# Performance work log

Measured on AMD Instinct MI355X. Metric: run time of the kernel, lower is better.

## Reference

```python
import jax, jax.numpy as jnp
import numpy as np

B, L, H, W_MAX, N_CLASSES = 32, 2048, 768, 512, 16


def setup_inputs() -> dict:
    key = jax.random.key(0)
    k_enc, k_len, k_w1, k_w2 = jax.random.split(key, 4)
    encoder_output = jax.random.normal(k_enc, (B, L, H), dtype=jnp.float32)
    # Ragged word spans: word lengths in [1, 8], consecutive spans via exclusive cumsum.
    lengths = jax.random.randint(k_len, (B, W_MAX), 1, 9)
    ends = jnp.cumsum(lengths, axis=1).astype(jnp.int32)
    starts = (ends - lengths).astype(jnp.int32)
    # Spans running past L become invalid (mask=0), matching the original's guard.
    W1 = jax.random.normal(k_w1, (H, H // 2), dtype=jnp.float32) * 0.02
    b1 = jnp.zeros((H // 2,), dtype=jnp.float32)
    W2 = jax.random.normal(k_w2, (H // 2, N_CLASSES), dtype=jnp.float32) * 0.02
    b2 = jnp.zeros((N_CLASSES,), dtype=jnp.float32)
    return {"encoder_output": encoder_output, "starts": starts, "ends": ends,
            "W1": W1, "b1": b1, "W2": W2, "b2": b2}


def reference(encoder_output, starts, ends, W1, b1, W2, b2):
    Bq, Lq, Hq = encoder_output.shape
    # Validity guard identical to original: s < L and e <= L and s < e
    valid = (starts < Lq) & (ends <= Lq) & (starts < ends)          # (B, W)
    mask = valid.astype(jnp.float32)
    # Prefix sums over sequence dim (zero-prepended): (B, L+1, H)
    csum = jnp.concatenate(
        [jnp.zeros((Bq, 1, Hq), encoder_output.dtype),
         jnp.cumsum(encoder_output, axis=1)], axis=1)
    s_idx = jnp.clip(starts, 0, Lq)[:, :, None]                      # (B, W, 1)
    e_idx = jnp.clip(ends, 0, Lq)[:, :, None]
    span_sum = (jnp.take_along_axis(csum, e_idx, axis=1)
                - jnp.take_along_axis(csum, s_idx, axis=1))          # (B, W, H)
    counts = jnp.maximum(ends - starts, 1).astype(encoder_output.dtype)[:, :, None]
    pooled = jnp.where(valid[:, :, None], span_sum / counts, 0.0)    # (B, W, H)
    # MLP head (dropout is identity in eval mode); torch GELU default = exact erf
    h = jax.nn.gelu(pooled @ W1 + b1, approximate=False)
    logits = h @ W2 + b2                                             # (B, W, n_classes)
    return logits, mask
```

## Files before the change

kernel.cpp:

```cpp
#include <hip/hip_runtime.h>
#include <hip/hip_bf16.h>

#define B_  32
#define L_  2048
#define H_  768
#define W_  512
#define NC_ 16
#define HH_ 384

typedef __attribute__((ext_vector_type(8))) __bf16 bf16x8;
typedef __attribute__((ext_vector_type(4))) float floatx4;

static __device__ __forceinline__ unsigned short f2bf(float x) {
    union { float f; unsigned u; } v; v.f = x;
    unsigned r = v.u + 0x7FFF + ((v.u >> 16) & 1);
    return (unsigned short)(r >> 16);
}

__global__ void k_convert_w1(const float* __restrict__ W1, unsigned short* __restrict__ w1t) {
    int idx = blockIdx.x * 256 + threadIdx.x;
    int n = idx / H_;
    int k = idx - n * H_;
    w1t[idx] = f2bf(W1[k * HH_ + n]);
}

__global__ void k_pool(const float* __restrict__ enc, const int* __restrict__ starts,
                       const int* __restrict__ ends, unsigned short* __restrict__ pooled,
                       float* __restrict__ mask) {
    int bw = blockIdx.x;
    int t  = threadIdx.x;
    int s = starts[bw], e = ends[bw];
    bool valid = (s < L_) && (e <= L_) && (s < e);
    float4 acc = make_float4(0.f, 0.f, 0.f, 0.f);
    if (valid) {
        int b = bw >> 9;
        const float4* base = (const float4*)(enc + (size_t)b * L_ * H_);
        float inv = 1.0f / (float)(e - s);
        for (int r = s; r < e; ++r) {
            float4 v = base[r * (H_ / 4) + t];
            acc.x += v.x; acc.y += v.y; acc.z += v.z; acc.w += v.w;
        }
        acc.x *= inv; acc.y *= inv; acc.z *= inv; acc.w *= inv;
    }
    ushort4 o;
    o.x = f2bf(acc.x); o.y = f2bf(acc.y); o.z = f2bf(acc.z); o.w = f2bf(acc.w);
    *(ushort4*)(pooled + (size_t)bw * H_ + t * 4) = o;
    if (t == 0) mask[bw] = valid ? 1.0f : 0.0f;
}

#define BM  64
#define BK  64
#define LDA 72
#define LDB 72
#define LDH 388

__global__ __launch_bounds__(512) void k_mlp(
    const unsigned short* __restrict__ pooled,
    const unsigned short* __restrict__ w1t,
    const float* __restrict__ b1,
    const float* __restrict__ W2,
    const float* __restrict__ b2,
    float* __restrict__ out)
{
    __shared__ float smem[BM * LDH];
    unsigned short* sA = (unsigned short*)smem;
    unsigned short* sB = (unsigned short*)smem + BM * LDA;

    const int tid  = threadIdx.x;
    const int wave = tid >> 6, lane = tid & 63;
    const int wm = wave >> 2, wn = wave & 3;
    const int lr = lane & 15, lk = lane >> 4;

    const int m0 = blockIdx.x * BM;

    floatx4 acc[2][6];
    #pragma unroll
    for (int i = 0; i < 2; ++i)
        #pragma unroll
        for (int j = 0; j < 6; ++j) acc[i][j] = {0.f, 0.f, 0.f, 0.f};

    const int srow = tid >> 3;
    const int sseg = (tid & 7) * 8;

    for (int kt = 0; kt < 12; ++kt) {
        const int k0 = kt * BK;
        {
            bf16x8 v = *(const bf16x8*)(pooled + (size_t)(m0 + srow) * H_ + k0 + sseg);
            *(bf16x8*)(sA + srow * LDA + sseg) = v;
        }
        #pragma unroll
        for (int p = 0; p < 6; ++p) {
            int nrow = srow + p * 64;
            bf16x8 v = *(const bf16x8*)(w1t + (size_t)nrow * H_ + k0 + sseg);
            *(bf16x8*)(sB + nrow * LDB + sseg) = v;
        }
        __syncthreads();
        #pragma unroll
        for (int kk = 0; kk < 2; ++kk) {
            bf16x8 af[2], bfr[6];
            #pragma unroll
            for (int mi = 0; mi < 2; ++mi)
                af[mi] = *(const bf16x8*)(sA + (wm * 32 + mi * 16 + lr) * LDA + kk * 32 + lk * 8);
            #pragma unroll
            for (int ni = 0; ni < 6; ++ni)
                bfr[ni] = *(const bf16x8*)(sB + (wn * 96 + ni * 16 + lr) * LDB + kk * 32 + lk * 8);
            #pragma unroll
            for (int mi = 0; mi < 2; ++mi)
                #pragma unroll
                for (int ni = 0; ni < 6; ++ni)
                    acc[mi][ni] = __builtin_amdgcn_mfma_f32_16x16x32_bf16(
                        af[mi], bfr[ni], acc[mi][ni], 0, 0, 0);
        }
        __syncthreads();
    }

    #pragma unroll
    for (int mi = 0; mi < 2; ++mi) {
        #pragma unroll
        for (int ni = 0; ni < 6; ++ni) {
            int col = wn * 96 + ni * 16 + lr;
            float bias = b1[col];
            #pragma unroll
            for (int r = 0; r < 4; ++r) {
                int row = wm * 32 + mi * 16 + lk * 4 + r;
                float x = acc[mi][ni][r] + bias;
                float g = 0.5f * x * (1.0f + erff(x * 0.70710678118654752f));
                smem[row * LDH + col] = g;
            }
        }
    }
    __syncthreads();

    const int r = tid >> 3;
    const int c = tid & 7;
    float s0 = b2[c], s1 = b2[c + 8];
    const float* hrow = smem + r * LDH;
    #pragma unroll 4
    for (int k = 0; k < HH_; ++k) {
        float hv = hrow[k];
        s0 += hv * W2[k * NC_ + c];
        s1 += hv * W2[k * NC_ + c + 8];
    }
    float* orow = out + (size_t)(m0 + r) * NC_;
    orow[c] = s0;
    orow[c + 8] = s1;
}

extern "C" void kernel_launch(void* const* d_in, const int* in_sizes, int n_in,
                              void* d_out, int out_size, void* d_ws, size_t ws_size,
                              hipStream_t stream) {
    const float* enc    = (const float*)d_in[0];
    const int*   starts = (const int*)d_in[1];
    const int*   ends   = (const int*)d_in[2];
    const float* W1     = (const float*)d_in[3];
    const float* b1     = (const float*)d_in[4];
    const float* W2     = (const float*)d_in[5];
    const float* b2     = (const float*)d_in[6];
    float* out = (float*)d_out;

    unsigned short* w1t    = (unsigned short*)d_ws;
    unsigned short* pooled = w1t + (size_t)HH_ * H_;
    float* mask = out + (size_t)B_ * W_ * NC_;

    hipLaunchKernelGGL(k_convert_w1, dim3((HH_ * H_) / 256), dim3(256), 0, stream, W1, w1t);
    hipLaunchKernelGGL(k_pool, dim3(B_ * W_), dim3(192), 0, stream, enc, starts, ends, pooled, mask);
    hipLaunchKernelGGL(k_mlp, dim3((B_ * W_) / BM), dim3(512), 0, stream, pooled, w1t, b1, W2, b2, out);
}
```

Baseline: 349.4 us.

## Fuse span pooling into MLP kernel and tile the W1 transpose

Measured after the change: 335.6 us. -3.9%, faster.

```diff
diff --git a/kernel.cpp b/kernel.cpp
--- a/kernel.cpp
+++ b/kernel.cpp
@@ -1,12 +1,18 @@
 #include <hip/hip_runtime.h>
 #include <hip/hip_bf16.h>
 
-#define B_  32
-#define L_  2048
-#define H_  768
-#define W_  512
-#define NC_ 16
-#define HH_ 384
+#define B_   32
+#define L_   2048
+#define H_   768
+#define W_   512
+#define NC_  16
+#define HH_  384
+#define NWORDS (B_ * W_)
+#define NLOGITS (NWORDS * NC_)
+
+#define BM    32
+#define LDA   776
+#define LDH   388
 
 typedef __attribute__((ext_vector_type(8))) __bf16 bf16x8;
 typedef __attribute__((ext_vector_type(4))) float floatx4;
@@ -17,45 +23,26 @@
     return (unsigned short)(r >> 16);
 }
 
-__global__ void k_convert_w1(const float* __restrict__ W1, unsigned short* __restrict__ w1t) {
-    int idx = blockIdx.x * 256 + threadIdx.x;
-    int n = idx / H_;
-    int k = idx - n * H_;
-    w1t[idx] = f2bf(W1[k * HH_ + n]);
+__global__ __launch_bounds__(256) void k_convert_w1(const float* __restrict__ W1,
+                                                    unsigned short* __restrict__ w1t) {
+    __shared__ unsigned short tile[64][65];
+    const int k0 = blockIdx.x * 64;
+    const int n0 = blockIdx.y * 64;
+    const int tx = threadIdx.x & 63;
+    const int ty = threadIdx.x >> 6;
+    #pragma unroll
+    for (int r = 0; r < 64; r += 4)
+        tile[r + ty][tx] = f2bf(W1[(size_t)(k0 + r + ty) * HH_ + n0 + tx]);
+    __syncthreads();
+    #pragma unroll
+    for (int r = 0; r < 64; r += 4)
+        w1t[(size_t)(n0 + r + ty) * H_ + k0 + tx] = tile[tx][r + ty];
 }
 
-__global__ void k_pool(const float* __restrict__ enc, const int* __restrict__ starts,
-                       const int* __restrict__ ends, unsigned short* __restrict__ pooled,
-                       float* __restrict__ mask) {
-    int bw = blockIdx.x;
-    int t  = threadIdx.x;
-    int s = starts[bw], e = ends[bw];
-    bool valid = (s < L_) && (e <= L_) && (s < e);
-    float4 acc = make_float4(0.f, 0.f, 0.f, 0.f);
-    if (valid) {
-        int b = bw >> 9;
-        const float4* base = (const float4*)(enc + (size_t)b * L_ * H_);
-        float inv = 1.0f / (float)(e - s);
-        for (int r = s; r < e; ++r) {
-            float4 v = base[r * (H_ / 4) + t];
-            acc.x += v.x; acc.y += v.y; acc.z += v.z; acc.w += v.w;
-        }
-        acc.x *= inv; acc.y *= inv; acc.z *= inv; acc.w *= inv;
-    }
-    ushort4 o;
-    o.x = f2bf(acc.x); o.y = f2bf(acc.y); o.z = f2bf(acc.z); o.w = f2bf(acc.w);
-    *(ushort4*)(pooled + (size_t)bw * H_ + t * 4) = o;
-    if (t == 0) mask[bw] = valid ? 1.0f : 0.0f;
-}
-
-#define BM  64
-#define BK  64
-#define LDA 72
-#define LDB 72
-#define LDH 388
-
-__global__ __launch_bounds__(512) void k_mlp(
-    const unsigned short* __restrict__ pooled,
+__global__ __launch_bounds__(512, 4) void k_fused(
+    const float* __restrict__ enc,
+    const int* __restrict__ starts,
+    const int* __restrict__ ends,
     const unsigned short* __restrict__ w1t,
     const float* __restrict__ b1,
     const float* __restrict__ W2,
@@ -64,86 +51,93 @@
 {
     __shared__ float smem[BM * LDH];
     unsigned short* sA = (unsigned short*)smem;
-    unsigned short* sB = (unsigned short*)smem + BM * LDA;
 
     const int tid  = threadIdx.x;
     const int wave = tid >> 6, lane = tid & 63;
-    const int wm = wave >> 2, wn = wave & 3;
+    const int m0 = blockIdx.x * BM;
+    const int b  = m0 >> 9;
+
+    #pragma unroll
+    for (int wi = 0; wi < 4; ++wi) {
+        const int wloc = wave * 4 + wi;
+        const int gw   = m0 + wloc;
+        const int s = starts[gw], e = ends[gw];
+        const int len = e - s;
+        const bool valid = (s < L_) && (e <= L_) && (s < e);
+        floatx4 a0 = {0.f,0.f,0.f,0.f}, a1 = a0, a2 = a0;
+        if (valid) {
+            const floatx4* p = (const floatx4*)(enc + ((size_t)b * L_ + s) * H_) + lane;
+            #pragma unroll
+            for (int r = 0; r < 8; ++r) {
+                if (r < len) { a0 += p[0]; a1 += p[64]; a2 += p[128]; }
+                p += H_ / 4;
+            }
+            const float inv = 1.0f / (float)len;
+            a0 *= inv; a1 *= inv; a2 *= inv;
+        }
+        unsigned short* dst = sA + wloc * LDA + lane * 4;
+        ushort4 o;
+        o.x=f2bf(a0[0]); o.y=f2bf(a0[1]); o.z=f2bf(a0[2]); o.w=f2bf(a0[3]); *(ushort4*)(dst)       = o;
+        o.x=f2bf(a1[0]); o.y=f2bf(a1[1]); o.z=f2bf(a1[2]); o.w=f2bf(a1[3]); *(ushort4*)(dst + 256) = o;
+        o.x=f2bf(a2[0]); o.y=f2bf(a2[1]); o.z=f2bf(a2[2]); o.w=f2bf(a2[3]); *(ushort4*)(dst + 512) = o;
+        if (lane == 0) out[NLOGITS + gw] = valid ? 1.0f : 0.0f;
+    }
+    __syncthreads();
+
     const int lr = lane & 15, lk = lane >> 4;
-
-    const int m0 = blockIdx.x * BM;
-
-    floatx4 acc[2][6];
+    floatx4 acc[2][3];
     #pragma unroll
     for (int i = 0; i < 2; ++i)
         #pragma unroll
-        for (int j = 0; j < 6; ++j) acc[i][j] = {0.f, 0.f, 0.f, 0.f};
+        for (int j = 0; j < 3; ++j) acc[i][j] = {0.f,0.f,0.f,0.f};
 
-    const int srow = tid >> 3;
-    const int sseg = (tid & 7) * 8;
-
-    for (int kt = 0; kt < 12; ++kt) {
-        const int k0 = kt * BK;
-        {
-            bf16x8 v = *(const bf16x8*)(pooled + (size_t)(m0 + srow) * H_ + k0 + sseg);
-            *(bf16x8*)(sA + srow * LDA + sseg) = v;
-        }
-        #pragma unroll
-        for (int p = 0; p < 6; ++p) {
-            int nrow = srow + p * 64;
-            bf16x8 v = *(const bf16x8*)(w1t + (size_t)nrow * H_ + k0 + sseg);
-            *(bf16x8*)(sB + nrow * LDB + sseg) = v;
-        }
-        __syncthreads();
-        #pragma unroll
-        for (int kk = 0; kk < 2; ++kk) {
-            bf16x8 af[2], bfr[6];
-            #pragma unroll
-            for (int mi = 0; mi < 2; ++mi)
-                af[mi] = *(const bf16x8*)(sA + (wm * 32 + mi * 16 + lr) * LDA + kk * 32 + lk * 8);
-            #pragma unroll
-            for (int ni = 0; ni < 6; ++ni)
-                bfr[ni] = *(const bf16x8*)(sB + (wn * 96 + ni * 16 + lr) * LDB + kk * 32 + lk * 8);
-            #pragma unroll
-            for (int mi = 0; mi < 2; ++mi)
-                #pragma unroll
-                for (int ni = 0; ni < 6; ++ni)
-                    acc[mi][ni] = __builtin_amdgcn_mfma_f32_16x16x32_bf16(
-                        af[mi], bfr[ni], acc[mi][ni], 0, 0, 0);
-        }
-        __syncthreads();
-    }
+    const unsigned short* sa0 = sA + lr * LDA + lk * 8;
+    const unsigned short* bp0 = w1t + (size_t)(wave * 48 +  0 + lr) * H_ + lk * 8;
+    const unsigned short* bp1 = w1t + (size_t)(wave * 48 + 16 + lr) * H_ + lk * 8;
+    const unsigned short* bp2 = w1t + (size_t)(wave * 48 + 32 + lr) * H_ + lk * 8;
 
     #pragma unroll
-    for (int mi = 0; mi < 2; ++mi) {
+    for (int kk = 0; kk < 24; ++kk) {
+        const int ko = kk * 32;
+        bf16x8 af0 = *(const bf16x8*)(sa0 + ko);
+        bf16x8 af1 = *(const bf16x8*)(sa0 + 16 * LDA + ko);
+        bf16x8 bf0 = *(const bf16x8*)(bp0 + ko);
+        bf16x8 bf1 = *(const bf16x8*)(bp1 + ko);
+        bf16x8 bf2 = *(const bf16x8*)(bp2 + ko);
+        acc[0][0] = __builtin_amdgcn_mfma_f32_16x16x32_bf16(af0, bf0, acc[0][0], 0, 0, 0);
+        acc[1][0] = __builtin_amdgcn_mfma_f32_16x16x32_bf16(af1, bf0, acc[1][0], 0, 0, 0);
+        acc[0][1] = __builtin_amdgcn_mfma_f32_16x16x32_bf16(af0, bf1, acc[0][1], 0, 0, 0);
+        acc[1][1] = __builtin_amdgcn_mfma_f32_16x16x32_bf16(af1, bf1, acc[1][1], 0, 0, 0);
+        acc[0][2] = __builtin_amdgcn_mfma_f32_16x16x32_bf16(af0, bf2, acc[0][2], 0, 0, 0);
+        acc[1][2] = __builtin_amdgcn_mfma_f32_16x16x32_bf16(af1, bf2, acc[1][2], 0, 0, 0);
+    }
+    __syncthreads();
+
+    #pragma unroll
+    for (int ni = 0; ni < 3; ++ni) {
+        const int col = wave * 48 + ni * 16 + lr;
+        const float bias = b1[col];
         #pragma unroll
-        for (int ni = 0; ni < 6; ++ni) {
-            int col = wn * 96 + ni * 16 + lr;
-            float bias = b1[col];
+        for (int mi = 0; mi < 2; ++mi) {
             #pragma unroll
             for (int r = 0; r < 4; ++r) {
-                int row = wm * 32 + mi * 16 + lk * 4 + r;
-                float x = acc[mi][ni][r] + bias;
-                float g = 0.5f * x * (1.0f + erff(x * 0.70710678118654752f));
+                const int row = mi * 16 + lk * 4 + r;
+                const float x = acc[mi][ni][r] + bias;
+                const float g = 0.5f * x * (1.0f + erff(x * 0.70710678118654752f));
                 smem[row * LDH + col] = g;
             }
         }
     }
     __syncthreads();
 
-    const int r = tid >> 3;
-    const int c = tid & 7;
-    float s0 = b2[c], s1 = b2[c + 8];
+    const int r = tid >> 4;
+    const int c = tid & 15;
+    float s = b2[c];
     const float* hrow = smem + r * LDH;
-    #pragma unroll 4
-    for (int k = 0; k < HH_; ++k) {
-        float hv = hrow[k];
-        s0 += hv * W2[k * NC_ + c];
-        s1 += hv * W2[k * NC_ + c + 8];
-    }
-    float* orow = out + (size_t)(m0 + r) * NC_;
-    orow[c] = s0;
-    orow[c + 8] = s1;
+    #pragma unroll 8
+    for (int k = 0; k < HH_; ++k)
+        s += hrow[k] * W2[k * NC_ + c];
+    out[(size_t)(m0 + r) * NC_ + c] = s;
 }
 
 extern "C" void kernel_launch(void* const* d_in, const int* in_sizes, int n_in,
@@ -158,11 +152,9 @@
     const float* b2     = (const float*)d_in[6];
     float* out = (float*)d_out;
 
-    unsigned short* w1t    = (unsigned short*)d_ws;
-    unsigned short* pooled = w1t + (size_t)HH_ * H_;
-    float* mask = out + (size_t)B_ * W_ * NC_;
+    unsigned short* w1t = (unsigned short*)d_ws;
 
-    hipLaunchKernelGGL(k_convert_w1, dim3((HH_ * H_) / 256), dim3(256), 0, stream, W1, w1t);
-    hipLaunchKernelGGL(k_pool, dim3(B_ * W_), dim3(192), 0, stream, enc, starts, ends, pooled, mask);
-    hipLaunchKernelGGL(k_mlp, dim3((B_ * W_) / BM), dim3(512), 0, stream, pooled, w1t, b1, W2, b2, out);
+    hipLaunchKernelGGL(k_convert_w1, dim3(H_ / 64, HH_ / 64), dim3(256), 0, stream, W1, w1t);
+    hipLaunchKernelGGL(k_fused, dim3(NWORDS / BM), dim3(512), 0, stream,
+                       enc, starts, ends, w1t, b1, W2, b2, out);
 }
```
